# Kernel tuning notes

Hardware: AMD Instinct MI355X
Metric: run time of the kernel (lower is better)

Reference implementation:

```python
import jax, jax.numpy as jnp
import numpy as np

D_MODEL = 1024
N_HEADS = 16
HEAD_DIM = D_MODEL // N_HEADS
MAX_REL = 16
SEQ = 1024
BATCH = 4


def _rel_embed(table, length_q, length_k):
    # table: [2*MAX_REL+1, head_dim] -> [lq, lk, head_dim]
    dist = jnp.arange(length_k)[None, :] - jnp.arange(length_q)[:, None]
    idx = jnp.clip(dist, -MAX_REL, MAX_REL) + MAX_REL
    return table[idx]


def setup_inputs() -> dict:
    key = jax.random.key(0)
    ks = jax.random.split(key, 16)
    s = 1.0 / np.sqrt(D_MODEL)
    inp = {
        "query": jax.random.normal(ks[0], (BATCH, SEQ, D_MODEL), jnp.float32),
        "key": jax.random.normal(ks[1], (BATCH, SEQ, D_MODEL), jnp.float32),
        "value": jax.random.normal(ks[2], (BATCH, SEQ, D_MODEL), jnp.float32),
        "mask": jnp.ones((BATCH, SEQ, SEQ), jnp.int32),
        "Wq": jax.random.normal(ks[3], (D_MODEL, D_MODEL), jnp.float32) * s,
        "bq": jnp.zeros((D_MODEL,), jnp.float32),
        "Wk": jax.random.normal(ks[4], (D_MODEL, D_MODEL), jnp.float32) * s,
        "bk": jnp.zeros((D_MODEL,), jnp.float32),
        "Wv": jax.random.normal(ks[5], (D_MODEL, D_MODEL), jnp.float32) * s,
        "bv": jnp.zeros((D_MODEL,), jnp.float32),
        "Wo": jax.random.normal(ks[6], (D_MODEL, D_MODEL), jnp.float32) * s,
        "bo": jnp.zeros((D_MODEL,), jnp.float32),
        "emb_k": jax.random.normal(ks[7], (2 * MAX_REL + 1, HEAD_DIM), jnp.float32) * 0.1,
        "emb_v": jax.random.normal(ks[8], (2 * MAX_REL + 1, HEAD_DIM), jnp.float32) * 0.1,
    }
    return inp


def reference(query, key, value, mask, Wq, bq, Wk, bk, Wv, bv, Wo, bo, emb_k, emb_v):
    B, lq, _ = query.shape
    H, hd = N_HEADS, HEAD_DIM
    scale = jnp.sqrt(jnp.asarray(hd, query.dtype))

    q = (query @ Wq.T + bq).reshape(B, lq, H, hd)   # [B,S,H,hd]
    k = (key @ Wk.T + bk).reshape(B, lq, H, hd)
    v = (value @ Wv.T + bv).reshape(B, lq, H, hd)

    # content-content term
    attn1 = jnp.einsum("bqhd,bkhd->bhqk", q, k)
    # content-position term: r_k2[q,k,d]
    r_k2 = _rel_embed(emb_k, lq, lq)               # [S,S,hd]
    attn2 = jnp.einsum("bqhd,qkd->bhqk", q, r_k2)

    attn = (attn1 + attn2) / scale
    attn = jnp.where(mask[:, None, :, :] == 0, -jnp.inf, attn)
    attn = jax.nn.softmax(attn, axis=-1)           # [B,H,S,S]

    weight1 = jnp.einsum("bhqk,bkhd->bhqd", attn, v)
    r_v2 = _rel_embed(emb_v, lq, lq)               # [S,S,hd]
    weight2 = jnp.einsum("bhqk,qkd->bhqd", attn, r_v2)

    x = (weight1 + weight2).transpose(0, 2, 1, 3).reshape(B, lq, H * hd)
    return x @ Wo.T + bo
```

## Files before the change

### kernel.cpp

```cpp
#include <hip/hip_runtime.h>
#include <math.h>

#define D_MODEL 1024
#define N_HEADS 16
#define HEAD_DIM 64
#define MAX_REL 16
#define SEQ 1024
#define BATCH 4

typedef _Float16 f16x8 __attribute__((ext_vector_type(8)));
typedef _Float16 f16x4 __attribute__((ext_vector_type(4)));
typedef _Float16 f16x2 __attribute__((ext_vector_type(2)));
typedef float f32x4 __attribute__((ext_vector_type(4)));
typedef unsigned long long u64;

__device__ __forceinline__ void gld_lds16(const _Float16* g, _Float16* l) {
    __builtin_amdgcn_global_load_lds(
        (const __attribute__((address_space(1))) void*)(uintptr_t)g,
        (__attribute__((address_space(3))) void*)(uintptr_t)l, 16, 0, 0);
}

__global__ __launch_bounds__(256) void mask_compress(
    const int* __restrict__ mask, u64* __restrict__ mbits, int n64)
{
    const int wid  = (blockIdx.x * 256 + threadIdx.x) >> 6;
    const int lane = threadIdx.x & 63;
    if (wid < n64) {
        const int vv = mask[(size_t)wid * 64 + lane];
        const u64 bal = __ballot(vv != 0);
        if (lane == 0) mbits[wid] = bal;
    }
}

__global__ __launch_bounds__(256) void cvt_all(
    const float* __restrict__ q, const float* __restrict__ k, const float* __restrict__ v,
    const float* __restrict__ Wq, const float* __restrict__ Wk,
    const float* __restrict__ Wv, const float* __restrict__ Wo,
    _Float16* __restrict__ qin, _Float16* __restrict__ kin, _Float16* __restrict__ vin,
    _Float16* __restrict__ wq, _Float16* __restrict__ wk,
    _Float16* __restrict__ wv, _Float16* __restrict__ wo)
{
    const size_t M1 = 1u << 20;
    size_t f = ((size_t)blockIdx.x * 256 + threadIdx.x) * 4;
    const float* src; _Float16* dst; size_t off;
    if (f < 4*M1)       { src = q; dst = qin; off = f; }
    else if (f < 8*M1)  { src = k; dst = kin; off = f - 4*M1; }
    else if (f < 12*M1) { src = v; dst = vin; off = f - 8*M1; }
    else {
        int u = (int)(f >> 20) - 12;
        src = (u==0)?Wq:(u==1)?Wk:(u==2)?Wv:Wo;
        dst = (u==0)?wq:(u==1)?wk:(u==2)?wv:wo;
        off = f & (M1 - 1);
    }
    float4 x = *(const float4*)(src + off);
    f16x4 h; h[0]=(_Float16)x.x; h[1]=(_Float16)x.y; h[2]=(_Float16)x.z; h[3]=(_Float16)x.w;
    *(f16x4*)(dst + off) = h;
}

#define TBM 128
#define TBN 128
#define TBK 64

template <typename CT>
__global__ __launch_bounds__(256) void gemm_f16async(
    const _Float16* A0, const _Float16* A1, const _Float16* A2,
    const _Float16* W0, const _Float16* W1, const _Float16* W2,
    const float* b0, const float* b1, const float* b2,
    CT* C0, CT* C1, CT* C2, int M, int N, int K)
{
    __shared__ _Float16 As[TBM * TBK];
    __shared__ _Float16 Ws[TBN * TBK];

    const int z = blockIdx.z;
    const _Float16* A = (z==0)?A0:(z==1)?A1:A2;
    const _Float16* W = (z==0)?W0:(z==1)?W1:W2;
    const float* bias = (z==0)?b0:(z==1)?b1:b2;
    CT* C = (z==0)?C0:(z==1)?C1:C2;

    const int tid = threadIdx.x;
    const int lane = tid & 63;
    const int w = tid >> 6;
    const int quad = lane >> 4;
    const int l16 = lane & 15;
    const int m0 = blockIdx.y * TBM;
    const int n0 = blockIdx.x * TBN;
    const int wm = (w & 1) * 64;
    const int wn = (w >> 1) * 64;

    int em[4], ek[4];
    #pragma unroll
    for (int i = 0; i < 4; ++i) {
        const int e = i * 256 + tid;
        em[i] = e >> 3;
        ek[i] = (e & 7) ^ (em[i] & 7);
    }

    f32x4 acc[4][4];
    #pragma unroll
    for (int i = 0; i < 4; ++i)
        #pragma unroll
        for (int j = 0; j < 4; ++j)
            acc[i][j] = (f32x4){0.f, 0.f, 0.f, 0.f};

    for (int kt = 0; kt < K; kt += TBK) {
        if (kt) __syncthreads();
        #pragma unroll
        for (int i = 0; i < 4; ++i) {
            const int e = i * 256 + tid;
            gld_lds16(A + (size_t)(m0 + em[i]) * K + kt + ek[i] * 8, &As[e * 8]);
        }
        #pragma unroll
        for (int i = 0; i < 4; ++i) {
            const int e = i * 256 + tid;
            gld_lds16(W + (size_t)(n0 + em[i]) * K + kt + ek[i] * 8, &Ws[e * 8]);
        }
        __syncthreads();

        #pragma unroll
        for (int ks = 0; ks < 2; ++ks) {
            const int k8 = ks * 4 + quad;
            f16x8 af[4], bf[4];
            #pragma unroll
            for (int i = 0; i < 4; ++i) {
                const int m = wm + i * 16 + l16;
                af[i] = *(const f16x8*)&As[m * 64 + ((k8 ^ (m & 7)) * 8)];
            }
            #pragma unroll
            for (int j = 0; j < 4; ++j) {
                const int n = wn + j * 16 + l16;
                bf[j] = *(const f16x8*)&Ws[n * 64 + ((k8 ^ (n & 7)) * 8)];
            }
            #pragma unroll
            for (int i = 0; i < 4; ++i)
                #pragma unroll
                for (int j = 0; j < 4; ++j)
                    acc[i][j] = __builtin_amdgcn_mfma_f32_16x16x32_f16(af[i], bf[j], acc[i][j], 0, 0, 0);
        }
    }

    const int cbase = n0 + wn + l16;
    const int rbase = m0 + wm + quad * 4;
    #pragma unroll
    for (int j = 0; j < 4; ++j) {
        const int col = cbase + j * 16;
        const float bv = bias[col];
        #pragma unroll
        for (int i = 0; i < 4; ++i) {
            #pragma unroll
            for (int r = 0; r < 4; ++r) {
                const int m = rbase + i * 16 + r;
                C[(size_t)m * N + col] = (CT)(acc[i][j][r] + bv);
            }
        }
    }
}

#define QT 64
#define KT 64
#define SP 72
#define EVP 40

__global__ __launch_bounds__(256) void attn_flash_mfma3(
    const _Float16* __restrict__ q, const _Float16* __restrict__ kg,
    const _Float16* __restrict__ v, const u64* __restrict__ mbits,
    const float* __restrict__ emb_k, const float* __restrict__ emb_v,
    _Float16* __restrict__ x)
{
    __shared__ _Float16 Ks[2][KT * SP];
    __shared__ _Float16 Vt[2][HEAD_DIM * SP];
    __shared__ _Float16 Ps[QT * SP];
    __shared__ _Float16 EvT[HEAD_DIM * EVP];
    __shared__ _Float16 pbh[QT * 33];
    __shared__ _Float16 bandh[QT * 33];

    const int qt = blockIdx.x, h = blockIdx.y, b = blockIdx.z;
    const int q0 = qt * QT;
    const int tid = threadIdx.x;
    const int lane = tid & 63;
    const int w = tid >> 6;
    const int quad = lane >> 4;
    const int l16 = lane & 15;
    const int qrow = w * 16 + quad * 4;

    const int sr = tid >> 2, sc = (tid & 3) * 16;
    const int vk = (tid & 31) * 2, vd = (tid >> 5) * 8;
    const int k8 = vk >> 3, klo = vk & 7;

    f16x8 qf[2];
    {
        const _Float16* qp = q + ((size_t)(b*SEQ + q0 + w*16 + l16))*D_MODEL + h*HEAD_DIM;
        qf[0] = *(const f16x8*)(qp + quad*8);
        qf[1] = *(const f16x8*)(qp + 32 + quad*8);
    }

    if (sr < 48) {
        #pragma unroll
        for (int c = 0; c < 16; ++c) {
            float val = (sr < 33) ? emb_k[sr*HEAD_DIM + sc + c] : 0.f;
            Ks[0][sr*SP + sc + c] = (_Float16)val;
        }
    }
    for (int idx = tid; idx < HEAD_DIM*EVP; idx += 256) {
        const int d = idx / EVP, j = idx % EVP;
        float val = (j < 32) ? emb_v[j*HEAD_DIM + d] : 0.f;
        EvT[d*EVP + j] = (_Float16)val;
    }
    for (int i = tid; i < QT*33; i += 256) bandh[i] = (_Float16)(-60000.f);
    __syncthreads();

    f32x4 accP[3];
    #pragma unroll
    for (int jt = 0; jt < 3; ++jt) accP[jt] = (f32x4){0.f,0.f,0.f,0.f};
    #pragma unroll
    for (int ks2 = 0; ks2 < 2; ++ks2) {
        const int ko = ks2*32 + quad*8;
        #pragma unroll
        for (int jt = 0; jt < 3; ++jt) {
            f16x8 bf = *(const f16x8*)&Ks[0][(jt*16 + l16)*SP + ko];
            accP[jt] = __builtin_amdgcn_mfma_f32_16x16x32_f16(qf[ks2], bf, accP[jt], 0, 0, 0);
        }
    }
    #pragma unroll
    for (int jt = 0; jt < 3; ++jt) {
        const int j = jt*16 + l16;
        if (j < 33) {
            #pragma unroll
            for (int r = 0; r < 4; ++r) pbh[(qrow + r)*33 + j] = (_Float16)accP[jt][r];
        }
    }
    float pb0r[4], pb32r[4];
    #pragma unroll
    for (int r = 0; r < 4; ++r) {
        pb0r[r]  = __shfl(accP[0][r], quad * 16);
        pb32r[r] = __shfl(accP[2][r], quad * 16);
    }
    __syncthreads();

    float m_r[4], l_r[4], rt_r[4];
    #pragma unroll
    for (int r = 0; r < 4; ++r) { m_r[r] = -1e30f; l_r[r] = 0.f; rt_r[r] = 0.f; }
    f32x4 accO[4];
    #pragma unroll
    for (int dt = 0; dt < 4; ++dt) accO[dt] = (f32x4){0.f,0.f,0.f,0.f};

    f16x8 kp0, kp1, vp0, vp1;

    {
        const _Float16* kp = kg + ((size_t)(b*SEQ + sr))*D_MODEL + h*HEAD_DIM + sc;
        kp0 = *(const f16x8*)(kp);
        kp1 = *(const f16x8*)(kp + 8);
        const _Float16* vp = v + ((size_t)(b*SEQ + vk))*D_MODEL + h*HEAD_DIM + vd;
        vp0 = *(const f16x8*)(vp);
        vp1 = *(const f16x8*)(vp + D_MODEL);
        *(f16x8*)&Ks[0][sr*SP + sc]     = kp0;
        *(f16x8*)&Ks[0][sr*SP + sc + 8] = kp1;
        #pragma unroll
        for (int i = 0; i < 8; ++i) {
            const int d = vd + i;
            const int xd = (d >> 3) & 7;
            f16x2 pr; pr[0] = vp0[i]; pr[1] = vp1[i];
            *(f16x2*)&Vt[0][d*SP + ((k8 ^ xd) << 3) + klo] = pr;
        }
    }
    __syncthreads();

    const float inv_scale = 0.125f;

    for (int t = 0; t < SEQ/KT; ++t) {
        const int buf = t & 1;
        const int k0 = t * KT;

        if (t + 1 < SEQ/KT) {
            const int kn = k0 + KT;
            const _Float16* kp = kg + ((size_t)(b*SEQ + kn + sr))*D_MODEL + h*HEAD_DIM + sc;
            kp0 = *(const f16x8*)(kp);
            kp1 = *(const f16x8*)(kp + 8);
            const _Float16* vp = v + ((size_t)(b*SEQ + kn + vk))*D_MODEL + h*HEAD_DIM + vd;
            vp0 = *(const f16x8*)(vp);
            vp1 = *(const f16x8*)(vp + D_MODEL);
        }

        u64 mw[4];
        {
            const u64* mb = mbits + ((size_t)(b*SEQ + q0 + qrow)) * (SEQ/64) + t;
            #pragma unroll
            for (int r = 0; r < 4; ++r) mw[r] = mb[(size_t)r * (SEQ/64)];
        }

        f32x4 accS[4];
        #pragma unroll
        for (int jt = 0; jt < 4; ++jt) accS[jt] = (f32x4){0.f,0.f,0.f,0.f};
        #pragma unroll
        for (int ks2 = 0; ks2 < 2; ++ks2) {
            const int ko = ks2*32 + quad*8;
            #pragma unroll
            for (int jt = 0; jt < 4; ++jt) {
                f16x8 bf = *(const f16x8*)&Ks[buf][(jt*16 + l16)*SP + ko];
                accS[jt] = __builtin_amdgcn_mfma_f32_16x16x32_f16(qf[ks2], bf, accS[jt], 0, 0, 0);
            }
        }

        const int kq = k0 - q0;
        const int mode = (kq <= -128) ? 0 : (kq >= 128 ? 2 : 1);

        float rmax[4] = {-1e30f,-1e30f,-1e30f,-1e30f};
        #pragma unroll
        for (int jt = 0; jt < 4; ++jt) {
            const int kl = jt*16 + l16;
            #pragma unroll
            for (int r = 0; r < 4; ++r) {
                float pv;
                if (mode == 0) pv = pb0r[r];
                else if (mode == 2) pv = pb32r[r];
                else {
                    int dk = (k0 + kl) - (q0 + qrow + r);
                    int ii = (dk < -MAX_REL ? -MAX_REL : (dk > MAX_REL ? MAX_REL : dk)) + MAX_REL;
                    pv = (float)pbh[(qrow + r)*33 + ii];
                }
                float s = (accS[jt][r] + pv) * inv_scale;
                if (!((mw[r] >> kl) & 1ull)) s = -1e30f;
                accS[jt][r] = s;
                rmax[r] = fmaxf(rmax[r], s);
            }
        }
        #pragma unroll
        for (int r = 0; r < 4; ++r) {
            #pragma unroll
            for (int d = 1; d < 16; d <<= 1)
                rmax[r] = fmaxf(rmax[r], __shfl_xor(rmax[r], d));
        }
        float alf[4];
        #pragma unroll
        for (int r = 0; r < 4; ++r) {
            const float mn = fmaxf(m_r[r], rmax[r]);
            alf[r] = __expf(m_r[r] - mn);
            m_r[r] = mn;
        }

        float rs[4] = {0,0,0,0}, rts[4] = {0,0,0,0};
        #pragma unroll
        for (int jt = 0; jt < 4; ++jt) {
            const int kl = jt*16 + l16;
            #pragma unroll
            for (int r = 0; r < 4; ++r) {
                const float s = accS[jt][r];
                const float p = __expf(s - m_r[r]);
                rs[r] += p;
                if (mode == 2) rts[r] += p;
                else if (mode == 1) {
                    int dk = (k0 + kl) - (q0 + qrow + r);
                    if (dk > MAX_REL) rts[r] += p;
                    else if (dk >= -MAX_REL) bandh[(qrow + r)*33 + dk + MAX_REL] = (_Float16)s;
                }
                Ps[(qrow + r)*SP + kl] = (_Float16)p;
            }
        }
        #pragma unroll
        for (int r = 0; r < 4; ++r) {
            #pragma unroll
            for (int d = 1; d < 16; d <<= 1) rs[r] += __shfl_xor(rs[r], d);
        }
        if (mode != 0) {
            #pragma unroll
            for (int r = 0; r < 4; ++r) {
                #pragma unroll
                for (int d = 1; d < 16; d <<= 1) rts[r] += __shfl_xor(rts[r], d);
            }
        }
        #pragma unroll
        for (int r = 0; r < 4; ++r) {
            l_r[r]  = l_r[r]  * alf[r] + rs[r];
            rt_r[r] = rt_r[r] * alf[r] + rts[r];
        }
        #pragma unroll
        for (int dt = 0; dt < 4; ++dt)
            #pragma unroll
            for (int r = 0; r < 4; ++r) accO[dt][r] *= alf[r];

        #pragma unroll
        for (int ks2 = 0; ks2 < 2; ++ks2) {
            const int ko = ks2*32 + quad*8;
            const int k8n = ks2*4 + quad;
            f16x8 pf = *(const f16x8*)&Ps[(w*16 + l16)*SP + ko];
            #pragma unroll
            for (int dt = 0; dt < 4; ++dt) {
                const int d = dt*16 + l16;
                const int xd = (d >> 3) & 7;
                f16x8 vf = *(const f16x8*)&Vt[buf][d*SP + ((k8n ^ xd) << 3)];
                accO[dt] = __builtin_amdgcn_mfma_f32_16x16x32_f16(pf, vf, accO[dt], 0, 0, 0);
            }
        }

        if (t + 1 < SEQ/KT) {
            const int nb = buf ^ 1;
            *(f16x8*)&Ks[nb][sr*SP + sc]     = kp0;
            *(f16x8*)&Ks[nb][sr*SP + sc + 8] = kp1;
            #pragma unroll
            for (int i = 0; i < 8; ++i) {
                const int d = vd + i;
                const int xd = (d >> 3) & 7;
                f16x2 pr; pr[0] = vp0[i]; pr[1] = vp1[i];
                *(f16x2*)&Vt[nb][d*SP + ((k8 ^ xd) << 3) + klo] = pr;
            }
        }
        __syncthreads();
    }

    float ej0[4], ej1[4], e32[4], bsp[4];
    #pragma unroll
    for (int r = 0; r < 4; ++r) {
        const int ql = qrow + r;
        ej0[r] = __expf((float)bandh[ql*33 + l16]      - m_r[r]);
        ej1[r] = __expf((float)bandh[ql*33 + 16 + l16] - m_r[r]);
        e32[r] = __expf((float)bandh[ql*33 + 32]       - m_r[r]);
        bsp[r] = ej0[r] + ej1[r];
    }
    #pragma unroll
    for (int r = 0; r < 4; ++r) {
        #pragma unroll
        for (int d = 1; d < 16; d <<= 1) bsp[r] += __shfl_xor(bsp[r], d);
    }
    #pragma unroll
    for (int r = 0; r < 4; ++r) {
        const int ql = qrow + r;
        const float Pl = l_r[r] - rt_r[r] - (bsp[r] + e32[r]);
        Ps[ql*SP + l16]      = (_Float16)((l16 == 0) ? (ej0[r] + Pl) : ej0[r]);
        Ps[ql*SP + 16 + l16] = (_Float16)ej1[r];
    }

    f32x4 accW[4];
    #pragma unroll
    for (int dt = 0; dt < 4; ++dt) accW[dt] = (f32x4){0.f,0.f,0.f,0.f};
    {
        f16x8 pf = *(const f16x8*)&Ps[(w*16 + l16)*SP + quad*8];
        #pragma unroll
        for (int dt = 0; dt < 4; ++dt) {
            f16x8 ef = *(const f16x8*)&EvT[(dt*16 + l16)*EVP + quad*8];
            accW[dt] = __builtin_amdgcn_mfma_f32_16x16x32_f16(pf, ef, accW[dt], 0, 0, 0);
        }
    }
    #pragma unroll
    for (int r = 0; r < 4; ++r) {
        const float p32 = e32[r] + rt_r[r];
        const float linv = 1.f / l_r[r];
        const int qg = q0 + qrow + r;
        #pragma unroll
        for (int dt = 0; dt < 4; ++dt) {
            const float w32 = emb_v[32*HEAD_DIM + dt*16 + l16];
            x[((size_t)(b*SEQ + qg))*D_MODEL + h*HEAD_DIM + dt*16 + l16] =
                (_Float16)((accO[dt][r] + accW[dt][r] + p32 * w32) * linv);
        }
    }
}

extern "C" void kernel_launch(void* const* d_in, const int* in_sizes, int n_in,
                              void* d_out, int out_size, void* d_ws, size_t ws_size,
                              hipStream_t stream) {
    const float* query = (const float*)d_in[0];
    const float* key   = (const float*)d_in[1];
    const float* value = (const float*)d_in[2];
    const int*   mask  = (const int*)d_in[3];
    const float* Wq = (const float*)d_in[4];
    const float* bq = (const float*)d_in[5];
    const float* Wk = (const float*)d_in[6];
    const float* bk = (const float*)d_in[7];
    const float* Wv = (const float*)d_in[8];
    const float* bv = (const float*)d_in[9];
    const float* Wo = (const float*)d_in[10];
    const float* bo = (const float*)d_in[11];
    const float* emb_k = (const float*)d_in[12];
    const float* emb_v = (const float*)d_in[13];
    float* out = (float*)d_out;

    const size_t M1 = 1u << 20;
    const size_t MD = (size_t)BATCH * SEQ * D_MODEL;
    _Float16* ws16 = (_Float16*)d_ws;
    _Float16* qin = ws16;
    _Float16* kin = ws16 + 4*M1;
    _Float16* vin = ws16 + 8*M1;
    _Float16* qp  = ws16 + 12*M1;
    _Float16* kp  = ws16 + 16*M1;
    _Float16* vp  = ws16 + 20*M1;
    _Float16* wq16 = ws16 + 24*M1;
    _Float16* wk16 = ws16 + 25*M1;
    _Float16* wv16 = ws16 + 26*M1;
    _Float16* wo16 = ws16 + 27*M1;
    u64* mbits = (u64*)(ws16 + 28*M1);
    _Float16* xh = qin;

    const int Mrows = BATCH * SEQ;
    const int n64 = BATCH * SEQ * (SEQ / 64);

    cvt_all<<<dim3(16384), dim3(256), 0, stream>>>(
        query, key, value, Wq, Wk, Wv, Wo,
        qin, kin, vin, wq16, wk16, wv16, wo16);

    mask_compress<<<dim3((n64*64)/256), dim3(256), 0, stream>>>(mask, mbits, n64);

    dim3 gQKV(D_MODEL / TBN, Mrows / TBM, 3), tB(256);
    gemm_f16async<_Float16><<<gQKV, tB, 0, stream>>>(
        qin, kin, vin, wq16, wk16, wv16, bq, bk, bv, qp, kp, vp,
        Mrows, D_MODEL, D_MODEL);

    dim3 gA(SEQ/QT, N_HEADS, BATCH);
    attn_flash_mfma3<<<gA, dim3(256), 0, stream>>>(qp, kp, vp, mbits, emb_k, emb_v, xh);

    dim3 gO(D_MODEL / TBN, Mrows / TBM, 1);
    gemm_f16async<float><<<gO, tB, 0, stream>>>(
        xh, xh, xh, wo16, wo16, wo16, bo, bo, bo, out, out, out,
        Mrows, D_MODEL, D_MODEL);
}
```

Baseline: 316.3 us.

## Load K fragments directly from global, use exp2 softmax with lazy rescaling

The attention kernel stops staging K tiles in shared memory and reads MFMA B-fragments for K straight from global memory, freeing LDS and adding an occupancy hint in the launch bounds. Scores are pre-scaled by log2(e)/sqrt(d) so the softmax can use exp2 directly. The online-softmax rescale is skipped when no row max increases, and a fast path drops per-element mask tests when the whole tile is unmasked. Embedding staging reuses the V buffer. In exchange, K reads now rely on cache hits with strided global loads instead of LDS reuse.

```diff
diff --git a/kernel.cpp b/kernel.cpp
--- a/kernel.cpp
+++ b/kernel.cpp
@@ -158,18 +158,17 @@
 #define QT 64
 #define KT 64
 #define SP 72
-#define EVP 40
-
-__global__ __launch_bounds__(256) void attn_flash_mfma3(
+#define EVW 32
+
+__global__ __launch_bounds__(256, 4) void attn_flash_mfma3(
     const _Float16* __restrict__ q, const _Float16* __restrict__ kg,
     const _Float16* __restrict__ v, const u64* __restrict__ mbits,
     const float* __restrict__ emb_k, const float* __restrict__ emb_v,
     _Float16* __restrict__ x)
 {
-    __shared__ _Float16 Ks[2][KT * SP];
     __shared__ _Float16 Vt[2][HEAD_DIM * SP];
     __shared__ _Float16 Ps[QT * SP];
-    __shared__ _Float16 EvT[HEAD_DIM * EVP];
+    __shared__ _Float16 EvT[HEAD_DIM * EVW];
     __shared__ _Float16 pbh[QT * 33];
     __shared__ _Float16 bandh[QT * 33];
 
@@ -186,6 +185,8 @@
     const int vk = (tid & 31) * 2, vd = (tid >> 5) * 8;
     const int k8 = vk >> 3, klo = vk & 7;
 
+    const float CS = 0.18033688011112042f;
+
     f16x8 qf[2];
     {
         const _Float16* qp = q + ((size_t)(b*SEQ + q0 + w*16 + l16))*D_MODEL + h*HEAD_DIM;
@@ -193,17 +194,24 @@
         qf[1] = *(const f16x8*)(qp + 32 + quad*8);
     }
 
+    f16x8 vp0, vp1;
+    {
+        const _Float16* vp = v + ((size_t)(b*SEQ + vk))*D_MODEL + h*HEAD_DIM + vd;
+        vp0 = *(const f16x8*)(vp);
+        vp1 = *(const f16x8*)(vp + D_MODEL);
+    }
+
+    _Float16* Es = &Vt[0][0];
     if (sr < 48) {
         #pragma unroll
         for (int c = 0; c < 16; ++c) {
             float val = (sr < 33) ? emb_k[sr*HEAD_DIM + sc + c] : 0.f;
-            Ks[0][sr*SP + sc + c] = (_Float16)val;
-        }
-    }
-    for (int idx = tid; idx < HEAD_DIM*EVP; idx += 256) {
-        const int d = idx / EVP, j = idx % EVP;
-        float val = (j < 32) ? emb_v[j*HEAD_DIM + d] : 0.f;
-        EvT[d*EVP + j] = (_Float16)val;
+            Es[sr*SP + sc + c] = (_Float16)val;
+        }
+    }
+    for (int idx = tid; idx < HEAD_DIM*EVW; idx += 256) {
+        const int d = idx >> 5, j = idx & 31;
+        EvT[d*EVW + j] = (_Float16)emb_v[j*HEAD_DIM + d];
     }
     for (int i = tid; i < QT*33; i += 256) bandh[i] = (_Float16)(-60000.f);
     __syncthreads();
@@ -216,7 +224,7 @@
         const int ko = ks2*32 + quad*8;
         #pragma unroll
         for (int jt = 0; jt < 3; ++jt) {
-            f16x8 bf = *(const f16x8*)&Ks[0][(jt*16 + l16)*SP + ko];
+            f16x8 bf = *(const f16x8*)&Es[(jt*16 + l16)*SP + ko];
             accP[jt] = __builtin_amdgcn_mfma_f32_16x16x32_f16(qf[ks2], bf, accP[jt], 0, 0, 0);
         }
     }
@@ -225,14 +233,23 @@
         const int j = jt*16 + l16;
         if (j < 33) {
             #pragma unroll
-            for (int r = 0; r < 4; ++r) pbh[(qrow + r)*33 + j] = (_Float16)accP[jt][r];
+            for (int r = 0; r < 4; ++r) pbh[(qrow + r)*33 + j] = (_Float16)(accP[jt][r] * CS);
         }
     }
     float pb0r[4], pb32r[4];
     #pragma unroll
     for (int r = 0; r < 4; ++r) {
-        pb0r[r]  = __shfl(accP[0][r], quad * 16);
-        pb32r[r] = __shfl(accP[2][r], quad * 16);
+        pb0r[r]  = __shfl(accP[0][r], quad * 16) * CS;
+        pb32r[r] = __shfl(accP[2][r], quad * 16) * CS;
+    }
+    __syncthreads();
+
+    #pragma unroll
+    for (int i = 0; i < 8; ++i) {
+        const int d = vd + i;
+        const int xd = (d >> 3) & 7;
+        f16x2 pr; pr[0] = vp0[i]; pr[1] = vp1[i];
+        *(f16x2*)&Vt[0][d*SP + ((k8 ^ xd) << 3) + klo] = pr;
     }
     __syncthreads();
 
@@ -242,40 +259,15 @@
     f32x4 accO[4];
     #pragma unroll
     for (int dt = 0; dt < 4; ++dt) accO[dt] = (f32x4){0.f,0.f,0.f,0.f};
-
-    f16x8 kp0, kp1, vp0, vp1;
-
-    {
-        const _Float16* kp = kg + ((size_t)(b*SEQ + sr))*D_MODEL + h*HEAD_DIM + sc;
-        kp0 = *(const f16x8*)(kp);
-        kp1 = *(const f16x8*)(kp + 8);
-        const _Float16* vp = v + ((size_t)(b*SEQ + vk))*D_MODEL + h*HEAD_DIM + vd;
-        vp0 = *(const f16x8*)(vp);
-        vp1 = *(const f16x8*)(vp + D_MODEL);
-        *(f16x8*)&Ks[0][sr*SP + sc]     = kp0;
-        *(f16x8*)&Ks[0][sr*SP + sc + 8] = kp1;
-        #pragma unroll
-        for (int i = 0; i < 8; ++i) {
-            const int d = vd + i;
-            const int xd = (d >> 3) & 7;
-            f16x2 pr; pr[0] = vp0[i]; pr[1] = vp1[i];
-            *(f16x2*)&Vt[0][d*SP + ((k8 ^ xd) << 3) + klo] = pr;
-        }
-    }
-    __syncthreads();
-
-    const float inv_scale = 0.125f;
 
     for (int t = 0; t < SEQ/KT; ++t) {
         const int buf = t & 1;
         const int k0 = t * KT;
+        const int kq = k0 - q0;
+        const int mode = (kq <= -128) ? 0 : (kq >= 128 ? 2 : 1);
 
         if (t + 1 < SEQ/KT) {
-            const int kn = k0 + KT;
-            const _Float16* kp = kg + ((size_t)(b*SEQ + kn + sr))*D_MODEL + h*HEAD_DIM + sc;
-            kp0 = *(const f16x8*)(kp);
-            kp1 = *(const f16x8*)(kp + 8);
-            const _Float16* vp = v + ((size_t)(b*SEQ + kn + vk))*D_MODEL + h*HEAD_DIM + vd;
+            const _Float16* vp = v + ((size_t)(b*SEQ + k0 + KT + vk))*D_MODEL + h*HEAD_DIM + vd;
             vp0 = *(const f16x8*)(vp);
             vp1 = *(const f16x8*)(vp + D_MODEL);
         }
@@ -290,92 +282,138 @@
         f32x4 accS[4];
         #pragma unroll
         for (int jt = 0; jt < 4; ++jt) accS[jt] = (f32x4){0.f,0.f,0.f,0.f};
-        #pragma unroll
-        for (int ks2 = 0; ks2 < 2; ++ks2) {
-            const int ko = ks2*32 + quad*8;
+        {
+            const _Float16* kb = kg + ((size_t)(b*SEQ + k0 + l16))*D_MODEL + h*HEAD_DIM;
+            #pragma unroll
+            for (int ks2 = 0; ks2 < 2; ++ks2) {
+                const int ko = ks2*32 + quad*8;
+                #pragma unroll
+                for (int jt = 0; jt < 4; ++jt) {
+                    f16x8 bf = *(const f16x8*)(kb + (size_t)(jt*16)*D_MODEL + ko);
+                    accS[jt] = __builtin_amdgcn_mfma_f32_16x16x32_f16(qf[ks2], bf, accS[jt], 0, 0, 0);
+                }
+            }
+        }
+
+        const bool fm = __all((mw[0] & mw[1] & mw[2] & mw[3]) == ~0ull) != 0;
+
+        float rmax[4] = {-1e30f,-1e30f,-1e30f,-1e30f};
+        if (mode != 1) {
+            float pc[4];
+            #pragma unroll
+            for (int r = 0; r < 4; ++r) pc[r] = (mode == 0) ? pb0r[r] : pb32r[r];
+            if (fm) {
+                #pragma unroll
+                for (int jt = 0; jt < 4; ++jt)
+                    #pragma unroll
+                    for (int r = 0; r < 4; ++r) {
+                        const float s = fmaf(accS[jt][r], CS, pc[r]);
+                        accS[jt][r] = s;
+                        rmax[r] = fmaxf(rmax[r], s);
+                    }
+            } else {
+                #pragma unroll
+                for (int jt = 0; jt < 4; ++jt) {
+                    const int kl = jt*16 + l16;
+                    #pragma unroll
+                    for (int r = 0; r < 4; ++r) {
+                        float s = fmaf(accS[jt][r], CS, pc[r]);
+                        if (!((mw[r] >> kl) & 1ull)) s = -1e30f;
+                        accS[jt][r] = s;
+                        rmax[r] = fmaxf(rmax[r], s);
+                    }
+                }
+            }
+        } else {
             #pragma unroll
             for (int jt = 0; jt < 4; ++jt) {
-                f16x8 bf = *(const f16x8*)&Ks[buf][(jt*16 + l16)*SP + ko];
-                accS[jt] = __builtin_amdgcn_mfma_f32_16x16x32_f16(qf[ks2], bf, accS[jt], 0, 0, 0);
-            }
-        }
-
-        const int kq = k0 - q0;
-        const int mode = (kq <= -128) ? 0 : (kq >= 128 ? 2 : 1);
-
-        float rmax[4] = {-1e30f,-1e30f,-1e30f,-1e30f};
-        #pragma unroll
-        for (int jt = 0; jt < 4; ++jt) {
-            const int kl = jt*16 + l16;
-            #pragma unroll
-            for (int r = 0; r < 4; ++r) {
-                float pv;
-                if (mode == 0) pv = pb0r[r];
-                else if (mode == 2) pv = pb32r[r];
-                else {
-                    int dk = (k0 + kl) - (q0 + qrow + r);
-                    int ii = (dk < -MAX_REL ? -MAX_REL : (dk > MAX_REL ? MAX_REL : dk)) + MAX_REL;
-                    pv = (float)pbh[(qrow + r)*33 + ii];
+                const int kl = jt*16 + l16;
+                #pragma unroll
+                for (int r = 0; r < 4; ++r) {
+                    const int dk = (k0 + kl) - (q0 + qrow + r);
+                    const int ii = (dk < -MAX_REL ? -MAX_REL : (dk > MAX_REL ? MAX_REL : dk)) + MAX_REL;
+                    float s = fmaf(accS[jt][r], CS, (float)pbh[(qrow + r)*33 + ii]);
+                    if (!((mw[r] >> kl) & 1ull)) s = -1e30f;
+                    accS[jt][r] = s;
+                    rmax[r] = fmaxf(rmax[r], s);
                 }
-                float s = (accS[jt][r] + pv) * inv_scale;
-                if (!((mw[r] >> kl) & 1ull)) s = -1e30f;
-                accS[jt][r] = s;
-                rmax[r] = fmaxf(rmax[r], s);
-            }
-        }
+            }
+        }
+
         #pragma unroll
         for (int r = 0; r < 4; ++r) {
             #pragma unroll
             for (int d = 1; d < 16; d <<= 1)
                 rmax[r] = fmaxf(rmax[r], __shfl_xor(rmax[r], d));
         }
-        float alf[4];
-        #pragma unroll
-        for (int r = 0; r < 4; ++r) {
-            const float mn = fmaxf(m_r[r], rmax[r]);
-            alf[r] = __expf(m_r[r] - mn);
-            m_r[r] = mn;
-        }
-
-        float rs[4] = {0,0,0,0}, rts[4] = {0,0,0,0};
-        #pragma unroll
-        for (int jt = 0; jt < 4; ++jt) {
-            const int kl = jt*16 + l16;
+
+        int nm = 0;
+        #pragma unroll
+        for (int r = 0; r < 4; ++r) nm |= (rmax[r] > m_r[r]) ? 1 : 0;
+        if (__any(nm)) {
             #pragma unroll
             for (int r = 0; r < 4; ++r) {
-                const float s = accS[jt][r];
-                const float p = __expf(s - m_r[r]);
-                rs[r] += p;
-                if (mode == 2) rts[r] += p;
-                else if (mode == 1) {
-                    int dk = (k0 + kl) - (q0 + qrow + r);
+                const float mn = fmaxf(m_r[r], rmax[r]);
+                const float a = __builtin_amdgcn_exp2f(m_r[r] - mn);
+                m_r[r] = mn;
+                l_r[r] *= a;
+                rt_r[r] *= a;
+                #pragma unroll
+                for (int dt = 0; dt < 4; ++dt) accO[dt][r] *= a;
+            }
+        }
+
+        float rs[4] = {0.f,0.f,0.f,0.f};
+        if (mode != 1) {
+            #pragma unroll
+            for (int jt = 0; jt < 4; ++jt) {
+                const int kl = jt*16 + l16;
+                #pragma unroll
+                for (int r = 0; r < 4; ++r) {
+                    const float p = __builtin_amdgcn_exp2f(accS[jt][r] - m_r[r]);
+                    rs[r] += p;
+                    Ps[(qrow + r)*SP + kl] = (_Float16)p;
+                }
+            }
+            #pragma unroll
+            for (int r = 0; r < 4; ++r) {
+                #pragma unroll
+                for (int d = 1; d < 16; d <<= 1) rs[r] += __shfl_xor(rs[r], d);
+            }
+            #pragma unroll
+            for (int r = 0; r < 4; ++r) {
+                l_r[r] += rs[r];
+                if (mode == 2) rt_r[r] += rs[r];
+            }
+        } else {
+            float rts[4] = {0.f,0.f,0.f,0.f};
+            #pragma unroll
+            for (int jt = 0; jt < 4; ++jt) {
+                const int kl = jt*16 + l16;
+                #pragma unroll
+                for (int r = 0; r < 4; ++r) {
+                    const float p = __builtin_amdgcn_exp2f(accS[jt][r] - m_r[r]);
+                    rs[r] += p;
+                    const int dk = (k0 + kl) - (q0 + qrow + r);
                     if (dk > MAX_REL) rts[r] += p;
-                    else if (dk >= -MAX_REL) bandh[(qrow + r)*33 + dk + MAX_REL] = (_Float16)s;
+                    else if (dk >= -MAX_REL) bandh[(qrow + r)*33 + dk + MAX_REL] = (_Float16)accS[jt][r];
+                    Ps[(qrow + r)*SP + kl] = (_Float16)p;
                 }
-                Ps[(qrow + r)*SP + kl] = (_Float16)p;
-            }
-        }
-        #pragma unroll
-        for (int r = 0; r < 4; ++r) {
-            #pragma unroll
-            for (int d = 1; d < 16; d <<= 1) rs[r] += __shfl_xor(rs[r], d);
-        }
-        if (mode != 0) {
+            }
             #pragma unroll
             for (int r = 0; r < 4; ++r) {
                 #pragma unroll
-                for (int d = 1; d < 16; d <<= 1) rts[r] += __shfl_xor(rts[r], d);
-            }
-        }
-        #pragma unroll
-        for (int r = 0; r < 4; ++r) {
-            l_r[r]  = l_r[r]  * alf[r] + rs[r];
-            rt_r[r] = rt_r[r] * alf[r] + rts[r];
-        }
-        #pragma unroll
-        for (int dt = 0; dt < 4; ++dt)
-            #pragma unroll
-            for (int r = 0; r < 4; ++r) accO[dt][r] *= alf[r];
+                for (int d = 1; d < 16; d <<= 1) {
+                    rs[r]  += __shfl_xor(rs[r],  d);
+                    rts[r] += __shfl_xor(rts[r], d);
+                }
+            }
+            #pragma unroll
+            for (int r = 0; r < 4; ++r) {
+                l_r[r]  += rs[r];
+                rt_r[r] += rts[r];
+            }
+        }
 
         #pragma unroll
         for (int ks2 = 0; ks2 < 2; ++ks2) {
@@ -393,8 +431,6 @@
 
         if (t + 1 < SEQ/KT) {
             const int nb = buf ^ 1;
-            *(f16x8*)&Ks[nb][sr*SP + sc]     = kp0;
-            *(f16x8*)&Ks[nb][sr*SP + sc + 8] = kp1;
             #pragma unroll
             for (int i = 0; i < 8; ++i) {
                 const int d = vd + i;
@@ -410,9 +446,9 @@
     #pragma unroll
     for (int r = 0; r < 4; ++r) {
         const int ql = qrow + r;
-        ej0[r] = __expf((float)bandh[ql*33 + l16]      - m_r[r]);
-        ej1[r] = __expf((float)bandh[ql*33 + 16 + l16] - m_r[r]);
-        e32[r] = __expf((float)bandh[ql*33 + 32]       - m_r[r]);
+        ej0[r] = __builtin_amdgcn_exp2f((float)bandh[ql*33 + l16]      - m_r[r]);
+        ej1[r] = __builtin_amdgcn_exp2f((float)bandh[ql*33 + 16 + l16] - m_r[r]);
+        e32[r] = __builtin_amdgcn_exp2f((float)bandh[ql*33 + 32]       - m_r[r]);
         bsp[r] = ej0[r] + ej1[r];
     }
     #pragma unroll
@@ -435,7 +471,7 @@
         f16x8 pf = *(const f16x8*)&Ps[(w*16 + l16)*SP + quad*8];
         #pragma unroll
         for (int dt = 0; dt < 4; ++dt) {
-            f16x8 ef = *(const f16x8*)&EvT[(dt*16 + l16)*EVP + quad*8];
+            f16x8 ef = *(const f16x8*)&EvT[(dt*16 + l16)*EVW + quad*8];
             accW[dt] = __builtin_amdgcn_mfma_f32_16x16x32_f16(pf, ef, accW[dt], 0, 0, 0);
         }
     }
@@ -473,7 +509,6 @@
     float* out = (float*)d_out;
 
     const size_t M1 = 1u << 20;
-    const size_t MD = (size_t)BATCH * SEQ * D_MODEL;
     _Float16* ws16 = (_Float16*)d_ws;
     _Float16* qin = ws16;
     _Float16* kin = ws16 + 4*M1;
```

Result: slower. 394.2 us (+24.7%).
